# Performance work log

Hardware: AMD Instinct MI355X
Metric: run time of the kernel (lower is better)

Reference implementation:

```python
import jax, jax.numpy as jnp
import numpy as np
from jax import lax

NX, NY, H = 128, 128, 1.0
N_ITER = 320          # ~2.5*(NX+NY): enough for one-cell-per-iter wavefront propagation
NUM_STATION = 24
NUM_EVENT = 2000
NUM_PICKS = 200000
INF = 1.0e6


def setup_inputs() -> dict:
    key = jax.random.key(0)
    ks = jax.random.split(key, 8)
    # velocities (km/s): vp ~ U[5,6], vs = vp/1.73 (Poisson solid)
    vp = 5.0 + jax.random.uniform(ks[0], (NX, NY), dtype=jnp.float32)
    vs = vp / 1.73
    scale = jnp.array([(NX - 1) * H, (NY - 1) * H, 0.0], dtype=jnp.float32)
    station_loc = jax.random.uniform(ks[1], (NUM_STATION, 3), dtype=jnp.float32) * scale
    event_loc = jax.random.uniform(ks[2], (NUM_EVENT, 3), dtype=jnp.float32) * scale
    event_time = jax.random.normal(ks[3], (NUM_EVENT, 1), dtype=jnp.float32)
    pick_station = jax.random.randint(ks[4], (NUM_PICKS,), 0, NUM_STATION)
    pick_phase = jax.random.randint(ks[5], (NUM_PICKS,), 0, 2)  # 0=P, 1=S
    pick_event = jax.random.randint(ks[6], (NUM_PICKS,), 0, NUM_EVENT)
    phase_time = 20.0 + jax.random.normal(ks[7], (NUM_PICKS,), dtype=jnp.float32)
    return dict(vp=vp, vs=vs, station_loc=station_loc, event_loc=event_loc,
                event_time=event_time, pick_station=pick_station,
                pick_phase=pick_phase, pick_event=pick_event, phase_time=phase_time)


def eikonal_solve(f, ix, iy):
    """2D eikonal |grad u| = f, point source at grid (ix,iy).
    Vectorized Jacobi iteration of the upwind Godunov local solver
    (same fixed point as the C++ fast-sweeping op)."""
    fh = f * H
    src = jnp.zeros((NX, NY), bool).at[ix, iy].set(True)
    u0 = jnp.where(src, 0.0, INF).astype(f.dtype)

    def body(u, _):
        up = jnp.pad(u, 1, constant_values=INF)
        a = jnp.minimum(up[:-2, 1:-1], up[2:, 1:-1])   # min x-neighbors
        b = jnp.minimum(up[1:-1, :-2], up[1:-1, 2:])   # min y-neighbors
        d = jnp.abs(a - b)
        one_sided = jnp.minimum(a, b) + fh
        two_sided = 0.5 * (a + b + jnp.sqrt(jnp.maximum(2.0 * fh * fh - d * d, 0.0)))
        cand = jnp.where(d >= fh, one_sided, two_sided)
        un = jnp.where(src, 0.0, jnp.minimum(u, cand))
        return un, None

    u, _ = lax.scan(body, u0, None, length=N_ITER)
    return u


def _forward(vp, vs, station_loc, event_loc, event_time,
             pick_station, pick_phase, pick_event, phase_time):
    # station grid indices: ix = round(station_x / h)
    ix = jnp.clip(jnp.round(station_loc[:, 0] / H), 0, NX - 1).astype(jnp.int32)
    iy = jnp.clip(jnp.round(station_loc[:, 1] / H), 0, NY - 1).astype(jnp.int32)
    solve_all = jax.vmap(eikonal_solve, in_axes=(None, 0, 0))
    Tp = solve_all(1.0 / vp, ix, iy)          # [S, NX, NY]
    Ts = solve_all(1.0 / vs, ix, iy)          # [S, NX, NY]
    T = jnp.stack([Tp, Ts])                    # [2, S, NX, NY]

    # bilinear interpolation of travel-time table at event locations (per pick)
    x = event_loc[pick_event, 0]
    y = event_loc[pick_event, 1]
    ir0 = jnp.clip(jnp.floor(x / H), 0, NX - 2).astype(jnp.int32)
    iz0 = jnp.clip(jnp.floor(y / H), 0, NY - 2).astype(jnp.int32)
    xc = jnp.clip(x, 0.0, (NX - 1) * H)
    yc = jnp.clip(y, 0.0, (NY - 1) * H)
    r0 = ir0.astype(xc.dtype) * H
    z0 = iz0.astype(yc.dtype) * H
    r1 = r0 + H
    z1 = z0 + H
    ph, st = pick_phase, pick_station
    Q00 = T[ph, st, ir0, iz0]
    Q01 = T[ph, st, ir0, iz0 + 1]
    Q10 = T[ph, st, ir0 + 1, iz0]
    Q11 = T[ph, st, ir0 + 1, iz0 + 1]
    tt = (Q00 * (r1 - xc) * (z1 - yc) + Q10 * (xc - r0) * (z1 - yc)
          + Q01 * (r1 - xc) * (yc - z0) + Q11 * (xc - r0) * (yc - z0)) / (H * H)

    at = event_time[pick_event, 0] + tt        # predicted arrival time, [NUM_PICKS]

    # loss = sum over (station, phase) groups of per-group MSE (matches groupby loop)
    gid = st * 2 + ph
    sq = (at - phase_time) ** 2
    sse = jax.ops.segment_sum(sq, gid, num_segments=2 * NUM_STATION)
    cnt = jax.ops.segment_sum(jnp.ones_like(sq), gid, num_segments=2 * NUM_STATION)
    loss = jnp.sum(sse / jnp.maximum(cnt, 1.0))
    return at, loss


def reference(vp, vs, station_loc, event_loc, event_time,
              pick_station, pick_phase, pick_event, phase_time):
    return _forward(vp, vs, station_loc, event_loc, event_time,
                    pick_station, pick_phase, pick_event, phase_time)
```

## Files before the change

kernel.cpp:

```cpp
#include <hip/hip_runtime.h>

#define NXg   128
#define NYg   128
#define NSTA  24
#define NPICK 200000
#define INFV  1.0e6f
#define TS    8
#define TG    16
#define MAXO  200

__device__ __forceinline__ float fsqrt_fast(float x) {
#if __has_builtin(__builtin_amdgcn_sqrtf)
  return __builtin_amdgcn_sqrtf(x);
#else
  float r; asm("v_sqrt_f32 %0, %1" : "=v"(r) : "v"(x)); return r;
#endif
}


template<int DR, int DC>
__device__ __forceinline__ void gs_pass(
    float (&u)[TS][TS], const float (&fh)[TS][TS], const float (&t2)[TS][TS],
    const float (&tpa)[TS], const float (&bta)[TS],
    const float (&lfa)[TS], const float (&rga)[TS], int &chg)
{
#pragma unroll
  for (int rr = 0; rr < TS; rr++) {
    const int r = (DR > 0) ? rr : (TS - 1 - rr);
#pragma unroll
    for (int cc = 0; cc < TS; cc++) {
      const int c = (DC > 0) ? cc : (TS - 1 - cc);
      const float up = (r == 0)      ? tpa[c] : u[r - 1][c];
      const float dn = (r == TS - 1) ? bta[c] : u[r + 1][c];
      const float lf = (c == 0)      ? lfa[r] : u[r][c - 1];
      const float rt = (c == TS - 1) ? rga[r] : u[r][c + 1];
      const float a  = fminf(up, dn);
      const float b  = fminf(lf, rt);
      const float dd = a - b;
      const float w  = fh[r][c];
      const float s  = __builtin_fmaf(-dd, dd, t2[r][c]);
      const float tw = 0.5f * ((a + b) + fsqrt_fast(s));
      const float on = fminf(a, b) + w;
      const float cand = (fabsf(dd) >= w) ? on : tw;
      const float old = u[r][c];
      chg |= (cand < old);
      u[r][c] = fminf(old, cand);
    }
  }
}

__global__ __launch_bounds__(256, 1) void eik_kernel(
    const float* __restrict__ vp, const float* __restrict__ vs,
    const float* __restrict__ station_loc, float* __restrict__ tab)
{
  __shared__ float eT[TG * TG][TS];
  __shared__ float eB[TG * TG][TS];
  __shared__ float eL[TG * TG][TS];
  __shared__ float eR[TG * TG][TS];
  __shared__ int flg[TG + 2][TG + 2];

  const int t    = threadIdx.x;
  const int wv   = t >> 6;
  const int lane = t & 63;
  const int ti = (wv >> 1) * 8 + (lane >> 3);
  const int tj = (wv & 1) * 8 + (lane & 7);
  const int tid = ti * TG + tj;
  const int fi = ti + 1, fj = tj + 1;

  const int blk = blockIdx.x;
  const int st = blk % NSTA;
  const int ph = blk / NSTA;
  const float* __restrict__ v = ph ? vs : vp;

  for (int i = t; i < (TG + 2) * (TG + 2); i += 256) {
    const int r = i / (TG + 2), c = i % (TG + 2);
    (&flg[0][0])[i] = (r >= 1 && r <= TG && c >= 1 && c <= TG) ? 1 : 0;
  }

  const float sx = station_loc[st * 3 + 0];
  const float sy = station_loc[st * 3 + 1];
  int ix = (int)rintf(sx); ix = ix < 0 ? 0 : (ix > NXg - 1 ? NXg - 1 : ix);
  int iy = (int)rintf(sy); iy = iy < 0 ? 0 : (iy > NYg - 1 ? NYg - 1 : iy);

  const int p = ((((wv >> 1) * 64 + 32) > ix) ? 0 : 2)
              | (((( wv & 1) * 64 + 32) > iy) ? 0 : 1);

  const int r0 = ti * TS, c0 = tj * TS;
  float u[TS][TS], fh[TS][TS], t2[TS][TS];
#pragma unroll
  for (int r = 0; r < TS; r++) {
    const float4 v0 = *reinterpret_cast<const float4*>(&v[(r0 + r) * NYg + c0]);
    const float4 v1 = *reinterpret_cast<const float4*>(&v[(r0 + r) * NYg + c0 + 4]);
    fh[r][0] = 1.0f / v0.x; fh[r][1] = 1.0f / v0.y;
    fh[r][2] = 1.0f / v0.z; fh[r][3] = 1.0f / v0.w;
    fh[r][4] = 1.0f / v1.x; fh[r][5] = 1.0f / v1.y;
    fh[r][6] = 1.0f / v1.z; fh[r][7] = 1.0f / v1.w;
#pragma unroll
    for (int c = 0; c < TS; c++) {
      t2[r][c] = (2.0f * fh[r][c]) * fh[r][c];
      u[r][c] = ((r0 + r) == ix && (c0 + c) == iy) ? 0.0f : INFV;
    }
  }

  auto publish = [&]() {
    *reinterpret_cast<float4*>(&eT[tid][0]) = make_float4(u[0][0], u[0][1], u[0][2], u[0][3]);
    *reinterpret_cast<float4*>(&eT[tid][4]) = make_float4(u[0][4], u[0][5], u[0][6], u[0][7]);
    *reinterpret_cast<float4*>(&eB[tid][0]) = make_float4(u[7][0], u[7][1], u[7][2], u[7][3]);
    *reinterpret_cast<float4*>(&eB[tid][4]) = make_float4(u[7][4], u[7][5], u[7][6], u[7][7]);
    *reinterpret_cast<float4*>(&eL[tid][0]) = make_float4(u[0][0], u[1][0], u[2][0], u[3][0]);
    *reinterpret_cast<float4*>(&eL[tid][4]) = make_float4(u[4][0], u[5][0], u[6][0], u[7][0]);
    *reinterpret_cast<float4*>(&eR[tid][0]) = make_float4(u[0][7], u[1][7], u[2][7], u[3][7]);
    *reinterpret_cast<float4*>(&eR[tid][4]) = make_float4(u[4][7], u[5][7], u[6][7], u[7][7]);
  };

  publish();
  __syncthreads();

  for (int outer = 0; outer < MAXO; outer++) {
    const int nb = flg[fi][fj]
                 | flg[fi - 1][fj] | flg[fi + 1][fj]
                 | flg[fi][fj - 1] | flg[fi][fj + 1];
    int chg = 0;
    if (__any(nb)) {
      float tpa[TS], bta[TS], lfa[TS], rga[TS];
      {
        float4 h0 = make_float4(INFV, INFV, INFV, INFV), h1 = h0;
        if (ti > 0) {
          h0 = *reinterpret_cast<const float4*>(&eB[tid - TG][0]);
          h1 = *reinterpret_cast<const float4*>(&eB[tid - TG][4]);
        }
        tpa[0] = h0.x; tpa[1] = h0.y; tpa[2] = h0.z; tpa[3] = h0.w;
        tpa[4] = h1.x; tpa[5] = h1.y; tpa[6] = h1.z; tpa[7] = h1.w;
      }
      {
        float4 h0 = make_float4(INFV, INFV, INFV, INFV), h1 = h0;
        if (ti < TG - 1) {
          h0 = *reinterpret_cast<const float4*>(&eT[tid + TG][0]);
          h1 = *reinterpret_cast<const float4*>(&eT[tid + TG][4]);
        }
        bta[0] = h0.x; bta[1] = h0.y; bta[2] = h0.z; bta[3] = h0.w;
        bta[4] = h1.x; bta[5] = h1.y; bta[6] = h1.z; bta[7] = h1.w;
      }
      {
        float4 h0 = make_float4(INFV, INFV, INFV, INFV), h1 = h0;
        if (tj > 0) {
          h0 = *reinterpret_cast<const float4*>(&eR[tid - 1][0]);
          h1 = *reinterpret_cast<const float4*>(&eR[tid - 1][4]);
        }
        lfa[0] = h0.x; lfa[1] = h0.y; lfa[2] = h0.z; lfa[3] = h0.w;
        lfa[4] = h1.x; lfa[5] = h1.y; lfa[6] = h1.z; lfa[7] = h1.w;
      }
      {
        float4 h0 = make_float4(INFV, INFV, INFV, INFV), h1 = h0;
        if (tj < TG - 1) {
          h0 = *reinterpret_cast<const float4*>(&eL[tid + 1][0]);
          h1 = *reinterpret_cast<const float4*>(&eL[tid + 1][4]);
        }
        rga[0] = h0.x; rga[1] = h0.y; rga[2] = h0.z; rga[3] = h0.w;
        rga[4] = h1.x; rga[5] = h1.y; rga[6] = h1.z; rga[7] = h1.w;
      }

      for (int k = 0; k < 4; ++k) {
        int ck = 0;
        switch (p ^ k) {
          case 0: gs_pass<+1, +1>(u, fh, t2, tpa, bta, lfa, rga, ck); break;
          case 1: gs_pass<+1, -1>(u, fh, t2, tpa, bta, lfa, rga, ck); break;
          case 2: gs_pass<-1, +1>(u, fh, t2, tpa, bta, lfa, rga, ck); break;
          default:gs_pass<-1, -1>(u, fh, t2, tpa, bta, lfa, rga, ck); break;
        }
        chg |= ck;
        if (!__any(ck)) break;
      }
    }

    __syncthreads();

    flg[fi][fj] = chg;
    if (chg) publish();

    if (!__syncthreads_or(chg)) break;
  }

  float* __restrict__ To = tab + (size_t)(ph * NSTA + st) * NXg * NYg;
#pragma unroll
  for (int r = 0; r < TS; r++) {
    *reinterpret_cast<float4*>(&To[(r0 + r) * NYg + c0]) =
        make_float4(u[r][0], u[r][1], u[r][2], u[r][3]);
    *reinterpret_cast<float4*>(&To[(r0 + r) * NYg + c0 + 4]) =
        make_float4(u[r][4], u[r][5], u[r][6], u[r][7]);
  }
}

__global__ void picks_kernel(
    const float* __restrict__ evloc, const float* __restrict__ evtime,
    const int* __restrict__ pst, const int* __restrict__ pph,
    const int* __restrict__ pev, const float* __restrict__ ptime,
    const float* __restrict__ tab, float* __restrict__ out,
    float* __restrict__ acc)
{
  __shared__ float lsse[2 * NSTA];
  __shared__ float lcnt[2 * NSTA];
  if (threadIdx.x < 2 * NSTA) { lsse[threadIdx.x] = 0.0f; lcnt[threadIdx.x] = 0.0f; }
  __syncthreads();

  int i = blockIdx.x * blockDim.x + threadIdx.x;
  if (i < NPICK) {
    int e = pev[i], s = pst[i], p = pph[i];
    float x = evloc[e * 3 + 0];
    float y = evloc[e * 3 + 1];
    int ir0 = (int)floorf(x); ir0 = ir0 < 0 ? 0 : (ir0 > NXg - 2 ? NXg - 2 : ir0);
    int iz0 = (int)floorf(y); iz0 = iz0 < 0 ? 0 : (iz0 > NYg - 2 ? NYg - 2 : iz0);
    float xc = fminf(fmaxf(x, 0.0f), (float)(NXg - 1));
    float yc = fminf(fmaxf(y, 0.0f), (float)(NYg - 1));
    float r0f = (float)ir0, z0f = (float)iz0;
    float r1 = r0f + 1.0f, z1 = z0f + 1.0f;

    const float* Tb = tab + (size_t)(p * NSTA + s) * NXg * NYg;
    float Q00 = Tb[ir0 * NYg + iz0];
    float Q01 = Tb[ir0 * NYg + iz0 + 1];
    float Q10 = Tb[(ir0 + 1) * NYg + iz0];
    float Q11 = Tb[(ir0 + 1) * NYg + iz0 + 1];
    float tt = Q00 * (r1 - xc) * (z1 - yc) + Q10 * (xc - r0f) * (z1 - yc)
             + Q01 * (r1 - xc) * (yc - z0f) + Q11 * (xc - r0f) * (yc - z0f);
    float at = evtime[e] + tt;
    out[i] = at;

    float dq = at - ptime[i];
    int g = s * 2 + p;
    atomicAdd(&lsse[g], dq * dq);
    atomicAdd(&lcnt[g], 1.0f);
  }
  __syncthreads();
  if (threadIdx.x < 2 * NSTA) {
    atomicAdd(&acc[threadIdx.x], lsse[threadIdx.x]);
    atomicAdd(&acc[2 * NSTA + threadIdx.x], lcnt[threadIdx.x]);
  }
}

__global__ void loss_kernel(const float* __restrict__ acc, float* __restrict__ out)
{
  int l = threadIdx.x;
  float v = 0.0f;
  if (l < 2 * NSTA) v = acc[l] / fmaxf(acc[2 * NSTA + l], 1.0f);
#pragma unroll
  for (int o = 32; o > 0; o >>= 1) v += __shfl_down(v, o, 64);
  if (l == 0) out[NPICK] = v;
}

extern "C" void kernel_launch(void* const* d_in, const int* in_sizes, int n_in,
                              void* d_out, int out_size, void* d_ws, size_t ws_size,
                              hipStream_t stream)
{
  const float* vp           = (const float*)d_in[0];
  const float* vs           = (const float*)d_in[1];
  const float* station_loc  = (const float*)d_in[2];
  const float* event_loc    = (const float*)d_in[3];
  const float* event_time   = (const float*)d_in[4];
  const int*   pick_station = (const int*)d_in[5];
  const int*   pick_phase   = (const int*)d_in[6];
  const int*   pick_event   = (const int*)d_in[7];
  const float* phase_time   = (const float*)d_in[8];

  float* out = (float*)d_out;
  float* acc = (float*)d_ws;
  float* tab = acc + 256;

  hipMemsetAsync(d_ws, 0, 96 * sizeof(float), stream);

  eik_kernel<<<2 * NSTA, 256, 0, stream>>>(vp, vs, station_loc, tab);

  picks_kernel<<<(NPICK + 255) / 256, 256, 0, stream>>>(
      event_loc, event_time, pick_station, pick_phase, pick_event, phase_time,
      tab, out, acc);

  loss_kernel<<<1, 64, 0, stream>>>(acc, out);
}
```

Baseline: 303.8 us.

## Double-buffer tile edge exchange to drop one barrier per outer iteration

Edge arrays and change flags are double-buffered, with INF-padded halo cells so neighbour reads need no bounds branches. Each outer iteration reads from one buffer and writes to the other, which removes the __syncthreads that previously separated reads from publishes. The cost is that every tile now publishes all four edges every iteration, not only changed tiles, and shared memory use roughly doubles.

```diff
diff --git a/kernel.cpp b/kernel.cpp
--- a/kernel.cpp
+++ b/kernel.cpp
@@ -7,6 +7,7 @@
 #define INFV  1.0e6f
 #define TS    8
 #define TG    16
+#define RD    (TG + 2)
 #define MAXO  200
 
 __device__ __forceinline__ float fsqrt_fast(float x) {
@@ -53,28 +54,37 @@
     const float* __restrict__ vp, const float* __restrict__ vs,
     const float* __restrict__ station_loc, float* __restrict__ tab)
 {
-  __shared__ float eT[TG * TG][TS];
-  __shared__ float eB[TG * TG][TS];
-  __shared__ float eL[TG * TG][TS];
-  __shared__ float eR[TG * TG][TS];
-  __shared__ int flg[TG + 2][TG + 2];
+  __shared__ float eT[2][RD * RD][TS];
+  __shared__ float eB[2][RD * RD][TS];
+  __shared__ float eL[2][RD * RD][TS];
+  __shared__ float eR[2][RD * RD][TS];
+  __shared__ int flg[2][RD][RD];
 
   const int t    = threadIdx.x;
   const int wv   = t >> 6;
   const int lane = t & 63;
   const int ti = (wv >> 1) * 8 + (lane >> 3);
   const int tj = (wv & 1) * 8 + (lane & 7);
-  const int tid = ti * TG + tj;
   const int fi = ti + 1, fj = tj + 1;
+  const int rid = fi * RD + fj;
 
   const int blk = blockIdx.x;
   const int st = blk % NSTA;
   const int ph = blk / NSTA;
   const float* __restrict__ v = ph ? vs : vp;
 
-  for (int i = t; i < (TG + 2) * (TG + 2); i += 256) {
-    const int r = i / (TG + 2), c = i % (TG + 2);
-    (&flg[0][0])[i] = (r >= 1 && r <= TG && c >= 1 && c <= TG) ? 1 : 0;
+  for (int i = t; i < 2 * RD * RD; i += 256) {
+    const int b = i / (RD * RD), rem = i % (RD * RD);
+    const float4 inf4 = make_float4(INFV, INFV, INFV, INFV);
+    *reinterpret_cast<float4*>(&eT[b][rem][0]) = inf4;
+    *reinterpret_cast<float4*>(&eT[b][rem][4]) = inf4;
+    *reinterpret_cast<float4*>(&eB[b][rem][0]) = inf4;
+    *reinterpret_cast<float4*>(&eB[b][rem][4]) = inf4;
+    *reinterpret_cast<float4*>(&eL[b][rem][0]) = inf4;
+    *reinterpret_cast<float4*>(&eL[b][rem][4]) = inf4;
+    *reinterpret_cast<float4*>(&eR[b][rem][0]) = inf4;
+    *reinterpret_cast<float4*>(&eR[b][rem][4]) = inf4;
+    flg[b][rem / RD][rem % RD] = 0;
   }
 
   const float sx = station_loc[st * 3 + 0];
@@ -102,60 +112,52 @@
     }
   }
 
-  auto publish = [&]() {
-    *reinterpret_cast<float4*>(&eT[tid][0]) = make_float4(u[0][0], u[0][1], u[0][2], u[0][3]);
-    *reinterpret_cast<float4*>(&eT[tid][4]) = make_float4(u[0][4], u[0][5], u[0][6], u[0][7]);
-    *reinterpret_cast<float4*>(&eB[tid][0]) = make_float4(u[7][0], u[7][1], u[7][2], u[7][3]);
-    *reinterpret_cast<float4*>(&eB[tid][4]) = make_float4(u[7][4], u[7][5], u[7][6], u[7][7]);
-    *reinterpret_cast<float4*>(&eL[tid][0]) = make_float4(u[0][0], u[1][0], u[2][0], u[3][0]);
-    *reinterpret_cast<float4*>(&eL[tid][4]) = make_float4(u[4][0], u[5][0], u[6][0], u[7][0]);
-    *reinterpret_cast<float4*>(&eR[tid][0]) = make_float4(u[0][7], u[1][7], u[2][7], u[3][7]);
-    *reinterpret_cast<float4*>(&eR[tid][4]) = make_float4(u[4][7], u[5][7], u[6][7], u[7][7]);
+  auto publish = [&](int pb) {
+    *reinterpret_cast<float4*>(&eT[pb][rid][0]) = make_float4(u[0][0], u[0][1], u[0][2], u[0][3]);
+    *reinterpret_cast<float4*>(&eT[pb][rid][4]) = make_float4(u[0][4], u[0][5], u[0][6], u[0][7]);
+    *reinterpret_cast<float4*>(&eB[pb][rid][0]) = make_float4(u[7][0], u[7][1], u[7][2], u[7][3]);
+    *reinterpret_cast<float4*>(&eB[pb][rid][4]) = make_float4(u[7][4], u[7][5], u[7][6], u[7][7]);
+    *reinterpret_cast<float4*>(&eL[pb][rid][0]) = make_float4(u[0][0], u[1][0], u[2][0], u[3][0]);
+    *reinterpret_cast<float4*>(&eL[pb][rid][4]) = make_float4(u[4][0], u[5][0], u[6][0], u[7][0]);
+    *reinterpret_cast<float4*>(&eR[pb][rid][0]) = make_float4(u[0][7], u[1][7], u[2][7], u[3][7]);
+    *reinterpret_cast<float4*>(&eR[pb][rid][4]) = make_float4(u[4][7], u[5][7], u[6][7], u[7][7]);
   };
 
-  publish();
+  publish(0);
+  flg[0][fi][fj] = 1;
   __syncthreads();
 
   for (int outer = 0; outer < MAXO; outer++) {
-    const int nb = flg[fi][fj]
-                 | flg[fi - 1][fj] | flg[fi + 1][fj]
-                 | flg[fi][fj - 1] | flg[fi][fj + 1];
+    const int rb = outer & 1;
+    const int wb = 1 - rb;
+
+    const int nb = flg[rb][fi][fj]
+                 | flg[rb][fi - 1][fj] | flg[rb][fi + 1][fj]
+                 | flg[rb][fi][fj - 1] | flg[rb][fi][fj + 1];
     int chg = 0;
     if (__any(nb)) {
       float tpa[TS], bta[TS], lfa[TS], rga[TS];
       {
-        float4 h0 = make_float4(INFV, INFV, INFV, INFV), h1 = h0;
-        if (ti > 0) {
-          h0 = *reinterpret_cast<const float4*>(&eB[tid - TG][0]);
-          h1 = *reinterpret_cast<const float4*>(&eB[tid - TG][4]);
-        }
+        const float4 h0 = *reinterpret_cast<const float4*>(&eB[rb][rid - RD][0]);
+        const float4 h1 = *reinterpret_cast<const float4*>(&eB[rb][rid - RD][4]);
         tpa[0] = h0.x; tpa[1] = h0.y; tpa[2] = h0.z; tpa[3] = h0.w;
         tpa[4] = h1.x; tpa[5] = h1.y; tpa[6] = h1.z; tpa[7] = h1.w;
       }
       {
-        float4 h0 = make_float4(INFV, INFV, INFV, INFV), h1 = h0;
-        if (ti < TG - 1) {
-          h0 = *reinterpret_cast<const float4*>(&eT[tid + TG][0]);
-          h1 = *reinterpret_cast<const float4*>(&eT[tid + TG][4]);
-        }
+        const float4 h0 = *reinterpret_cast<const float4*>(&eT[rb][rid + RD][0]);
+        const float4 h1 = *reinterpret_cast<const float4*>(&eT[rb][rid + RD][4]);
         bta[0] = h0.x; bta[1] = h0.y; bta[2] = h0.z; bta[3] = h0.w;
         bta[4] = h1.x; bta[5] = h1.y; bta[6] = h1.z; bta[7] = h1.w;
       }
       {
-        float4 h0 = make_float4(INFV, INFV, INFV, INFV), h1 = h0;
-        if (tj > 0) {
-          h0 = *reinterpret_cast<const float4*>(&eR[tid - 1][0]);
-          h1 = *reinterpret_cast<const float4*>(&eR[tid - 1][4]);
-        }
+        const float4 h0 = *reinterpret_cast<const float4*>(&eR[rb][rid - 1][0]);
+        const float4 h1 = *reinterpret_cast<const float4*>(&eR[rb][rid - 1][4]);
         lfa[0] = h0.x; lfa[1] = h0.y; lfa[2] = h0.z; lfa[3] = h0.w;
         lfa[4] = h1.x; lfa[5] = h1.y; lfa[6] = h1.z; lfa[7] = h1.w;
       }
       {
-        float4 h0 = make_float4(INFV, INFV, INFV, INFV), h1 = h0;
-        if (tj < TG - 1) {
-          h0 = *reinterpret_cast<const float4*>(&eL[tid + 1][0]);
-          h1 = *reinterpret_cast<const float4*>(&eL[tid + 1][4]);
-        }
+        const float4 h0 = *reinterpret_cast<const float4*>(&eL[rb][rid + 1][0]);
+        const float4 h1 = *reinterpret_cast<const float4*>(&eL[rb][rid + 1][4]);
         rga[0] = h0.x; rga[1] = h0.y; rga[2] = h0.z; rga[3] = h0.w;
         rga[4] = h1.x; rga[5] = h1.y; rga[6] = h1.z; rga[7] = h1.w;
       }
@@ -173,10 +175,8 @@
       }
     }
 
-    __syncthreads();
-
-    flg[fi][fj] = chg;
-    if (chg) publish();
+    publish(wb);
+    flg[wb][fi][fj] = chg;
 
     if (!__syncthreads_or(chg)) break;
   }
```

New measurement: 298.5 us (median of 2 runs). About the same (-1.7%).
